# Kernel optimization log

Hardware: AMD Instinct MI355X
Metric: run time of the kernel (lower is better)

The kernel has to match this reference:

```python
import jax, jax.numpy as jnp
import numpy as np

H = 256          # hidden_channels
R = 64           # num_rbf
N = 20000        # nodes
E = 320000       # edges
CUTOFF_LO = 0.0
CUTOFF_UP = 5.0
LN_EPS = 1e-5


def _layernorm(x, g, b):
    mu = jnp.mean(x, axis=-1, keepdims=True)
    var = jnp.var(x, axis=-1, keepdims=True)
    return (x - mu) * jax.lax.rsqrt(var + LN_EPS) * g + b


def _cosine_cutoff(r):
    # cutoff_lower == 0 branch of CosineCutoff
    c = 0.5 * (jnp.cos(r * (jnp.pi / CUTOFF_UP)) + 1.0)
    return c * (r < CUTOFF_UP).astype(r.dtype)


def setup_inputs() -> dict:
    key = jax.random.key(0)
    ks = jax.random.split(key, 16)
    def xavier(k, shape):
        fan_in, fan_out = shape[1], shape[0]
        lim = np.sqrt(6.0 / (fan_in + fan_out))
        return jax.random.uniform(k, shape, jnp.float32, -lim, lim)
    x = jax.random.normal(ks[0], (N, H), jnp.float32)
    edge_index = jax.random.randint(ks[1], (2, E), 0, N, jnp.int64)
    edge_weight = jax.random.uniform(ks[2], (E,), jnp.float32, 0.0, CUTOFF_UP)
    edge_attr = jax.random.normal(ks[3], (E, R), jnp.float32)
    return {
        "x": x,
        "edge_index": edge_index,
        "edge_weight": edge_weight,
        "edge_attr": edge_attr,
        "ln_g": jnp.ones((H,), jnp.float32),
        "ln_b": jnp.zeros((H,), jnp.float32),
        "Wq": xavier(ks[4], (H, H)), "bq": jnp.zeros((H,), jnp.float32),
        "Wk": xavier(ks[5], (H, H)), "bk": jnp.zeros((H,), jnp.float32),
        "Wv": xavier(ks[6], (H, H)), "bv": jnp.zeros((H,), jnp.float32),
        "Wo": xavier(ks[7], (H, H)), "bo": jnp.zeros((H,), jnp.float32),
        "Wdk": xavier(ks[8], (H, R)), "bdk": jnp.zeros((H,), jnp.float32),
        "Wdv": xavier(ks[9], (H, R)), "bdv": jnp.zeros((H,), jnp.float32),
    }


def reference(x, edge_index, edge_weight, edge_attr,
              ln_g, ln_b, Wq, bq, Wk, bk, Wv, bv, Wo, bo, Wdk, bdk, Wdv, bdv):
    src = edge_index[0]  # j (messages come from)
    dst = edge_index[1]  # i (messages aggregate to)

    x_norm = _layernorm(x, ln_g, ln_b)                     # [N,H]
    q = x_norm @ Wq.T + bq                                 # [N,H]
    k = x_norm @ Wk.T + bk
    v = x_norm @ Wv.T + bv

    dk = jax.nn.silu(edge_attr @ Wdk.T + bdk)              # [E,H]
    dv = jax.nn.silu(edge_attr @ Wdv.T + bdv)              # [E,H]

    q_i = q[dst]                                           # [E,H]
    k_j = k[src]
    v_j = v[src]

    attn = jnp.sum(q_i * k_j * dk, axis=1)                 # [E]
    attn = jax.nn.silu(attn) * _cosine_cutoff(edge_weight) # [E]

    msg = v_j * dv * attn[:, None]                         # [E,H]
    agg = jax.ops.segment_sum(msg, dst, num_segments=x.shape[0])  # [N,H]

    out = agg @ Wo.T + bo
    return x + out
```

## Files before the change

### kernel.cpp

```cpp
#include <hip/hip_runtime.h>
#include <math.h>

#define NN 20000
#define H 256
#define R 64
#define EE 320000
#define LN_EPS 1e-5f
#define NB 79

using short8  = __attribute__((ext_vector_type(8))) short;
using ushort8 = __attribute__((ext_vector_type(8))) unsigned short;
using f32x4   = __attribute__((ext_vector_type(4))) float;

typedef __attribute__((address_space(3))) unsigned int lds_uint;
typedef const __attribute__((address_space(1))) unsigned int glb_uint;

__device__ __forceinline__ float silu_f(float x) {
    return x * __builtin_amdgcn_rcpf(1.0f + __expf(-x));
}

__device__ __forceinline__ unsigned short f2bf(float f) {
    unsigned u = __float_as_uint(f);
    u += 0x7fff + ((u >> 16) & 1);
    return (unsigned short)(u >> 16);
}
__device__ __forceinline__ float bf2f(unsigned short s) {
    return __uint_as_float(((unsigned)s) << 16);
}
__device__ __forceinline__ unsigned short f2h(float f) {
    unsigned r;
    asm("v_cvt_f16_f32 %0, %1" : "=v"(r) : "v"(f));
    return (unsigned short)r;
}
__device__ __forceinline__ float h2f(unsigned short h) {
    float f;
    asm("v_cvt_f32_f16 %0, %1" : "=v"(f) : "v"((unsigned)h));
    return f;
}

__device__ __forceinline__ int sw_idx(int row, int col) {
    return row * 64 + ((((col >> 3) ^ (row & 7)) << 3) | (col & 7));
}
__device__ __forceinline__ int dh_idx(int row, int col) {
    return row * 256 + (col ^ (((row >> 2) & 3) << 4));
}

__global__ __launch_bounds__(256) void k_prep(
    const float* __restrict__ Wq, const float* __restrict__ Wk,
    const float* __restrict__ Wv, const float* __restrict__ Wo,
    const float* __restrict__ g,  const float* __restrict__ b,
    const float* __restrict__ bq, const float* __restrict__ bk, const float* __restrict__ bv,
    const float* __restrict__ Wdk, const float* __restrict__ Wdv,
    unsigned short* __restrict__ wqkv_p, unsigned short* __restrict__ wo_p,
    unsigned short* __restrict__ wdk_p,  unsigned short* __restrict__ wdv_p,
    float* __restrict__ bias3, int* __restrict__ hist)
{
    const int bid = blockIdx.x, t = threadIdx.x;
    if (bid < 128) {
        const int mat = bid >> 5;
        const float* W = mat == 0 ? Wq : (mat == 1 ? Wk : (mat == 2 ? Wv : Wo));
        unsigned short* out = (mat < 3) ? wqkv_p + (size_t)mat * 131072 : wo_p;
        const int fold = mat < 3;
        const int flat = (bid & 31) * 256 + t;
        const int tile = flat >> 9;
        const int rem  = flat & 511;
        const int ks   = rem >> 6;
        const int lane = rem & 63;
        const int nl = lane & 15, quad = lane >> 4;
        const int h  = tile * 16 + nl;
        const int c0 = ks * 32 + quad * 8;
        short8 hi8, lo8;
        #pragma unroll
        for (int j = 0; j < 8; ++j) {
            float wv = W[(size_t)h * 256 + c0 + j];
            if (fold) wv *= g[c0 + j];
            const unsigned short hh = f2bf(wv);
            hi8[j] = (short)hh;
            lo8[j] = (short)f2bf(wv - bf2f(hh));
        }
        unsigned short* ob = out + ((size_t)(tile * 8 + ks)) * 1024;
        *(short8*)&ob[lane * 8] = hi8;
        *(short8*)&ob[512 + lane * 8] = lo8;
    } else if (bid < 160) {
        const int flat = (bid - 128) * 256 + t;
        const int mat  = flat >> 12;
        const int rem  = flat & 4095;
        const int hh   = rem >> 11;
        const int r2   = rem & 2047;
        const int row  = r2 >> 4;
        const int col4 = (r2 & 15) * 4;
        const float* W = mat == 0 ? Wdk : Wdv;
        unsigned short* out = (mat == 0 ? wdk_p : wdv_p) + hh * 16384;
        const float4 w4 = *(const float4*)(W + (size_t)(hh * 128 + row) * 64 + col4);
        const unsigned short h0 = f2bf(w4.x), h1 = f2bf(w4.y), h2 = f2bf(w4.z), h3 = f2bf(w4.w);
        ushort4 hi4 = {h0, h1, h2, h3};
        ushort4 lo4 = {f2bf(w4.x - bf2f(h0)), f2bf(w4.y - bf2f(h1)),
                       f2bf(w4.z - bf2f(h2)), f2bf(w4.w - bf2f(h3))};
        const int di = sw_idx(row, col4);
        *(ushort4*)&out[di] = hi4;
        *(ushort4*)&out[8192 + di] = lo4;
    } else if (bid < 163) {
        const int mat = bid - 160, h = t;
        const float* W  = mat == 0 ? Wq : (mat == 1 ? Wk : Wv);
        const float* bb = mat == 0 ? bq : (mat == 1 ? bk : bv);
        float s = 0.f;
        const float* wr = W + (size_t)h * 256;
        for (int c = 0; c < 256; c += 4) {
            const float4 w4 = *(const float4*)(wr + c);
            const float4 b4 = *(const float4*)(b + c);
            s += w4.x * b4.x + w4.y * b4.y + w4.z * b4.z + w4.w * b4.w;
        }
        bias3[mat * 256 + h] = bb[h] + s;
    } else {
        const int i = (bid - 163) * 256 + t;
        if (i < NN) hist[i] = 0;
    }
}

__global__ __launch_bounds__(64, 2) void k_ln_qkv(
    const float* __restrict__ x,
    const unsigned short* __restrict__ wqkv_p, const float* __restrict__ bias3,
    float* __restrict__ q, float* __restrict__ k, float* __restrict__ v)
{
    const int t = threadIdx.x;
    const int lane = t & 63;
    const int nl = lane & 15, quad = lane >> 4;
    const int nbase = blockIdx.x * 16;
    const int node = nbase + nl;
    const bool nv = node < NN;

    float xv[64];
    float sum = 0.f, sq = 0.f;
    {
        const float* xp = x + (size_t)node * H + quad * 8;
        #pragma unroll
        for (int ks = 0; ks < 8; ++ks) {
            float4 x0 = {0.f,0.f,0.f,0.f}, x1 = {0.f,0.f,0.f,0.f};
            if (nv) {
                x0 = *(const float4*)(xp + ks * 32);
                x1 = *(const float4*)(xp + ks * 32 + 4);
            }
            xv[ks*8+0]=x0.x; xv[ks*8+1]=x0.y; xv[ks*8+2]=x0.z; xv[ks*8+3]=x0.w;
            xv[ks*8+4]=x1.x; xv[ks*8+5]=x1.y; xv[ks*8+6]=x1.z; xv[ks*8+7]=x1.w;
            sum += x0.x+x0.y+x0.z+x0.w + x1.x+x1.y+x1.z+x1.w;
            sq  += x0.x*x0.x+x0.y*x0.y+x0.z*x0.z+x0.w*x0.w
                 + x1.x*x1.x+x1.y*x1.y+x1.z*x1.z+x1.w*x1.w;
        }
    }
    sum += __shfl_xor(sum, 16); sum += __shfl_xor(sum, 32);
    sq  += __shfl_xor(sq, 16);  sq  += __shfl_xor(sq, 32);
    const float mu  = sum * (1.0f / H);
    const float var = sq * (1.0f / H) - mu * mu;
    const float rs  = rsqrtf(var + LN_EPS);

    short8 a_hi[8], a_lo[8];
    #pragma unroll
    for (int ks = 0; ks < 8; ++ks) {
        #pragma unroll
        for (int j = 0; j < 8; ++j) {
            const float z = (xv[ks*8+j] - mu) * rs;
            const unsigned short hh = f2bf(z);
            a_hi[ks][j] = (short)hh;
            a_lo[ks][j] = (short)f2bf(z - bf2f(hh));
        }
    }

    for (int mat = 0; mat < 3; ++mat) {
        float* outp = mat == 0 ? q : (mat == 1 ? k : v);
        const float* bp = bias3 + mat * 256;
        const unsigned short* wb = wqkv_p + (size_t)mat * 131072 + lane * 8;
        for (int tile = 0; tile < 16; ++tile) {
            const unsigned short* gb = wb + (size_t)tile * 8192;
            const float bbv = bp[tile * 16 + nl];
            f32x4 acc = {bbv, bbv, bbv, bbv};
            #pragma unroll
            for (int ks = 0; ks < 8; ++ks) {
                const short8 b_hi = *(const short8*)(gb + ks * 1024);
                const short8 b_lo = *(const short8*)(gb + ks * 1024 + 512);
                acc = __builtin_amdgcn_mfma_f32_16x16x32_bf16(a_hi[ks], b_hi, acc, 0, 0, 0);
                acc = __builtin_amdgcn_mfma_f32_16x16x32_bf16(a_lo[ks], b_hi, acc, 0, 0, 0);
                acc = __builtin_amdgcn_mfma_f32_16x16x32_bf16(a_hi[ks], b_lo, acc, 0, 0, 0);
            }
            #pragma unroll
            for (int r = 0; r < 4; ++r) {
                const int onode = nbase + quad * 4 + r;
                if (onode < NN)
                    outp[(size_t)onode * H + tile * 16 + nl] = acc[r];
            }
        }
    }
}

__global__ __launch_bounds__(256) void k_hist(const int* __restrict__ ei, int* __restrict__ hist) {
    int e = blockIdx.x * 256 + threadIdx.x;
    if (e < EE) atomicAdd(&hist[ei[EE + e]], 1);
}

__global__ __launch_bounds__(256) void k_scan1(const int* __restrict__ hist,
                                               int* __restrict__ cursor, int* __restrict__ bsum) {
    const int t = threadIdx.x, i = blockIdx.x * 256 + t;
    const int lane = t & 63, w = t >> 6;
    const int v = (i < NN) ? hist[i] : 0;
    int incl = v;
    #pragma unroll
    for (int off = 1; off < 64; off <<= 1) {
        int u = __shfl_up(incl, off);
        if (lane >= off) incl += u;
    }
    __shared__ int ws[4];
    if (lane == 63) ws[w] = incl;
    __syncthreads();
    int base = 0;
    #pragma unroll
    for (int j = 0; j < 4; ++j) if (j < w) base += ws[j];
    if (i < NN) cursor[i] = base + incl - v;
    if (t == 255) bsum[blockIdx.x] = base + incl;
}

__global__ __launch_bounds__(128) void k_scan2(int* __restrict__ bsum) {
    __shared__ int buf[128];
    const int t = threadIdx.x;
    const int v = (t < NB) ? bsum[t] : 0;
    buf[t] = v;
    __syncthreads();
    #pragma unroll
    for (int off = 1; off < 128; off <<= 1) {
        int add = (t >= off) ? buf[t - off] : 0;
        __syncthreads();
        buf[t] += add;
        __syncthreads();
    }
    if (t < NB) bsum[t] = buf[t] - v;
}

__global__ __launch_bounds__(256) void k_scatter(const int* __restrict__ ei,
                                                 int* __restrict__ cursor,
                                                 const int* __restrict__ bsum,
                                                 int* __restrict__ perm) {
    int e = blockIdx.x * 256 + threadIdx.x;
    if (e < EE) {
        int d = ei[EE + e];
        int pos = atomicAdd(&cursor[d], 1) + bsum[d >> 8];
        perm[pos] = e;
    }
}

__global__ __launch_bounds__(256, 2) void k_edge(
    const float* __restrict__ q, const float* __restrict__ k, const float* __restrict__ v,
    const int* __restrict__ ei, const float* __restrict__ ew, const float* __restrict__ ea,
    const unsigned short* __restrict__ wdk_p, const float* __restrict__ bdk,
    const unsigned short* __restrict__ wdv_p, const float* __restrict__ bdv,
    const int* __restrict__ perm,
    float* __restrict__ agg)
{
    __shared__ __align__(16) unsigned short w_region[2 * 128 * 64];
    __shared__ __align__(16) unsigned short dks_h[64 * 256];
    __shared__ float attn_s[64];
    __shared__ int src_s[64], dst_s[64];

    const unsigned short* w_hi_s = w_region;
    const unsigned short* w_lo_s = w_region + 128 * 64;

    const int t    = threadIdx.x;
    const int bi   = blockIdx.x;
    const int eb   = ((bi & 7) * 625 + (bi >> 3)) * 64;
    const int lane = t & 63, wave = t >> 6;
    const int nl   = lane & 15, quad = lane >> 4;
    const int estrip = wave * 16;
    const int tx = t & 31, ty = t >> 5;
    const int h0 = tx * 4, e0 = ty * 8;

    {
        const ushort8* sp = (const ushort8*)wdk_p + t;
        ushort8* dpw = (ushort8*)w_region + (t & 192);
        #pragma unroll
        for (int c = 0; c < 8; ++c)
            __builtin_amdgcn_global_load_lds((glb_uint*)(sp + c * 256),
                                             (lds_uint*)(dpw + c * 256), 16, 0, 0);
    }

    if (t < 64) {
        const int e = perm[eb + t];
        src_s[t] = ei[e];
        dst_s[t] = ei[EE + e];
        attn_s[t] = 0.f;
    }

    short8 a_hi[2], a_lo[2];
    {
        const int e = perm[eb + estrip + nl];
        const float* ap = ea + (size_t)e * R + quad * 8;
        #pragma unroll
        for (int ks = 0; ks < 2; ++ks) {
            const f32x4 x0 = *(const f32x4*)(ap + ks * 32);
            const f32x4 x1 = *(const f32x4*)(ap + ks * 32 + 4);
            const float zz[8] = {x0[0], x0[1], x0[2], x0[3], x1[0], x1[1], x1[2], x1[3]};
            #pragma unroll
            for (int j = 0; j < 8; ++j) {
                const unsigned short hv = f2bf(zz[j]);
                a_hi[ks][j] = (short)hv;
                a_lo[ks][j] = (short)f2bf(zz[j] - bf2f(hv));
            }
        }
    }
    __syncthreads();

    #define MFMA_TO_DKS(BIAS, HALF)                                                   \
    {                                                                                 \
        f32x4 accA[8];                                                                \
        _Pragma("unroll")                                                             \
        for (int tt = 0; tt < 8; ++tt) {                                              \
            const int wrow = tt * 16 + nl;                                            \
            short8 b_hi[2], b_lo[2];                                                  \
            _Pragma("unroll")                                                         \
            for (int ks = 0; ks < 2; ++ks) {                                          \
                const int idx = wrow * 64 + ((((ks * 4 + quad) ^ (nl & 7)) << 3));    \
                b_hi[ks] = *(const short8*)&w_hi_s[idx];                              \
                b_lo[ks] = *(const short8*)&w_lo_s[idx];                              \
            }                                                                         \
            const float bb = (BIAS)[(HALF) * 128 + tt * 16 + nl];                     \
            f32x4 acc = {bb, bb, bb, bb};                                             \
            _Pragma("unroll")                                                         \
            for (int ks = 0; ks < 2; ++ks) {                                          \
                acc = __builtin_amdgcn_mfma_f32_16x16x32_bf16(a_hi[ks], b_hi[ks], acc, 0, 0, 0); \
                acc = __builtin_amdgcn_mfma_f32_16x16x32_bf16(a_lo[ks], b_hi[ks], acc, 0, 0, 0); \
                acc = __builtin_amdgcn_mfma_f32_16x16x32_bf16(a_hi[ks], b_lo[ks], acc, 0, 0, 0); \
            }                                                                         \
            accA[tt] = acc;                                                           \
        }                                                                             \
        __syncthreads();                         \
                   \
        _Pragma("unroll")                                                             \
        for (int tt = 0; tt < 8; ++tt)                                                \
            _Pragma("unroll")                                                         \
            for (int r = 0; r < 4; ++r)                                               \
                dks_h[dh_idx(estrip + quad * 4 + r, (HALF) * 128 + tt * 16 + nl)] =   \
                    f2h(silu_f(accA[tt][r]));                                         \
    }

    #define STAGE(PTR)                                                                \
    {                                                                                 \
        const ushort8* sp = (const ushort8*)(PTR) + t;                                \
        ushort8* dpw = (ushort8*)w_region + (t & 192);                                \
        _Pragma("unroll")                                                             \
        for (int c = 0; c < 8; ++c)                                                   \
            __builtin_amdgcn_global_load_lds((glb_uint*)(sp + c * 256),               \
                                             (lds_uint*)(dpw + c * 256), 16, 0, 0);   \
    }

    {
        f32x4 accA[8];
        #pragma unroll
        for (int tt = 0; tt < 8; ++tt) {
            const int wrow = tt * 16 + nl;
            short8 b_hi[2], b_lo[2];
            #pragma unroll
            for (int ks = 0; ks < 2; ++ks) {
                const int idx = wrow * 64 + ((((ks * 4 + quad) ^ (nl & 7)) << 3));
                b_hi[ks] = *(const short8*)&w_hi_s[idx];
                b_lo[ks] = *(const short8*)&w_lo_s[idx];
            }
            const float bb = bdk[tt * 16 + nl];
            f32x4 acc = {bb, bb, bb, bb};
            #pragma unroll
            for (int ks = 0; ks < 2; ++ks) {
                acc = __builtin_amdgcn_mfma_f32_16x16x32_bf16(a_hi[ks], b_hi[ks], acc, 0, 0, 0);
                acc = __builtin_amdgcn_mfma_f32_16x16x32_bf16(a_lo[ks], b_hi[ks], acc, 0, 0, 0);
                acc = __builtin_amdgcn_mfma_f32_16x16x32_bf16(a_hi[ks], b_lo[ks], acc, 0, 0, 0);
            }
            accA[tt] = acc;
        }
        __syncthreads();
        STAGE(wdk_p + 16384);
        #pragma unroll
        for (int tt = 0; tt < 8; ++tt)
            #pragma unroll
            for (int r = 0; r < 4; ++r)
                dks_h[dh_idx(estrip + quad * 4 + r, tt * 16 + nl)] =
                    f2h(silu_f(accA[tt][r]));
    }
    __syncthreads();
    MFMA_TO_DKS(bdk, 1);
    STAGE(wdv_p);

    {
        float4 qi0 = {0.f,0.f,0.f,0.f}, qi1 = {0.f,0.f,0.f,0.f};
        int pd = -1;
        #pragma unroll
        for (int i = 0; i < 8; ++i) {
            const int d = dst_s[e0 + i], s = src_s[e0 + i];
            if (d != pd) {
                qi0 = *(const float4*)(q + (size_t)d * H + h0);
                qi1 = *(const float4*)(q + (size_t)d * H + 128 + h0);
                pd = d;
            }
            const float4 kj0 = *(const float4*)(k + (size_t)s * H + h0);
            const float4 kj1 = *(const float4*)(k + (size_t)s * H + 128 + h0);
            const ushort4 d40 = *(const ushort4*)&dks_h[dh_idx(e0 + i, h0)];
            const ushort4 d41 = *(const ushort4*)&dks_h[dh_idx(e0 + i, 128 + h0)];
            float part = qi0.x * kj0.x * h2f(d40.x) + qi0.y * kj0.y * h2f(d40.y)
                       + qi0.z * kj0.z * h2f(d40.z) + qi0.w * kj0.w * h2f(d40.w)
                       + qi1.x * kj1.x * h2f(d41.x) + qi1.y * kj1.y * h2f(d41.y)
                       + qi1.z * kj1.z * h2f(d41.z) + qi1.w * kj1.w * h2f(d41.w);
            #pragma unroll
            for (int off = 16; off; off >>= 1) part += __shfl_xor(part, off);
            if (tx == 0) attn_s[e0 + i] += part;
        }
    }
    __syncthreads();

    if (t < 64) {
        const int e = perm[eb + t];
        const float rr = ew[e];
        const float cut = (rr < 5.0f) ? 0.5f * (__cosf(rr * 0.6283185307f) + 1.0f) : 0.0f;
        attn_s[t] = silu_f(attn_s[t]) * cut;
    }

    MFMA_TO_DKS(bdv, 0);
    STAGE(wdv_p + 16384);
    __syncthreads();
    MFMA_TO_DKS(bdv, 1);

    {
        float4 m0 = {0.f,0.f,0.f,0.f}, m1 = {0.f,0.f,0.f,0.f};
        int cur_d = -1;
        #pragma unroll
        for (int i = 0; i < 8; ++i) {
            const int d = dst_s[e0 + i], s = src_s[e0 + i];
            const float a = attn_s[e0 + i];
            const float4 vj0 = *(const float4*)(v + (size_t)s * H + h0);
            const float4 vj1 = *(const float4*)(v + (size_t)s * H + 128 + h0);
            const ushort4 d40 = *(const ushort4*)&dks_h[dh_idx(e0 + i, h0)];
            const ushort4 d41 = *(const ushort4*)&dks_h[dh_idx(e0 + i, 128 + h0)];
            if (d != cur_d) {
                if (cur_d >= 0) {
                    float* dp = agg + (size_t)cur_d * H;
                    atomicAdd(dp + h0 + 0, m0.x); atomicAdd(dp + h0 + 1, m0.y);
                    atomicAdd(dp + h0 + 2, m0.z); atomicAdd(dp + h0 + 3, m0.w);
                    atomicAdd(dp + 128 + h0 + 0, m1.x); atomicAdd(dp + 128 + h0 + 1, m1.y);
                    atomicAdd(dp + 128 + h0 + 2, m1.z); atomicAdd(dp + 128 + h0 + 3, m1.w);
                }
                m0.x = vj0.x * h2f(d40.x) * a; m0.y = vj0.y * h2f(d40.y) * a;
                m0.z = vj0.z * h2f(d40.z) * a; m0.w = vj0.w * h2f(d40.w) * a;
                m1.x = vj1.x * h2f(d41.x) * a; m1.y = vj1.y * h2f(d41.y) * a;
                m1.z = vj1.z * h2f(d41.z) * a; m1.w = vj1.w * h2f(d41.w) * a;
                cur_d = d;
            } else {
                m0.x += vj0.x * h2f(d40.x) * a; m0.y += vj0.y * h2f(d40.y) * a;
                m0.z += vj0.z * h2f(d40.z) * a; m0.w += vj0.w * h2f(d40.w) * a;
                m1.x += vj1.x * h2f(d41.x) * a; m1.y += vj1.y * h2f(d41.y) * a;
                m1.z += vj1.z * h2f(d41.z) * a; m1.w += vj1.w * h2f(d41.w) * a;
            }
        }
        {
            float* dp = agg + (size_t)cur_d * H;
            atomicAdd(dp + h0 + 0, m0.x); atomicAdd(dp + h0 + 1, m0.y);
            atomicAdd(dp + h0 + 2, m0.z); atomicAdd(dp + h0 + 3, m0.w);
            atomicAdd(dp + 128 + h0 + 0, m1.x); atomicAdd(dp + 128 + h0 + 1, m1.y);
            atomicAdd(dp + 128 + h0 + 2, m1.z); atomicAdd(dp + 128 + h0 + 3, m1.w);
        }
    }
    #undef MFMA_TO_DKS
    #undef STAGE
}

__global__ __launch_bounds__(64, 2) void k_out(
    const float* __restrict__ aggm, const unsigned short* __restrict__ wo_p,
    const float* __restrict__ bo, const float* __restrict__ x, float* __restrict__ out)
{
    const int t = threadIdx.x;
    const int lane = t & 63;
    const int nl = lane & 15, quad = lane >> 4;
    const int nbase = blockIdx.x * 16;
    const int node = nbase + nl;
    const bool nv = node < NN;

    short8 a_hi[8], a_lo[8];
    {
        const float* ap = aggm + (size_t)node * H + quad * 8;
        #pragma unroll
        for (int ks = 0; ks < 8; ++ks) {
            float4 x0 = {0.f,0.f,0.f,0.f}, x1 = {0.f,0.f,0.f,0.f};
            if (nv) { x0 = *(const float4*)(ap + ks * 32); x1 = *(const float4*)(ap + ks * 32 + 4); }
            const float zz[8] = {x0.x,x0.y,x0.z,x0.w,x1.x,x1.y,x1.z,x1.w};
            #pragma unroll
            for (int j = 0; j < 8; ++j) {
                const unsigned short hh = f2bf(zz[j]);
                a_hi[ks][j] = (short)hh;
                a_lo[ks][j] = (short)f2bf(zz[j] - bf2f(hh));
            }
        }
    }
    for (int tile = 0; tile < 16; ++tile) {
        const unsigned short* gb = wo_p + (size_t)tile * 8192 + lane * 8;
        const float bbv = bo[tile * 16 + nl];
        f32x4 acc = {bbv, bbv, bbv, bbv};
        #pragma unroll
        for (int ks = 0; ks < 8; ++ks) {
            const short8 b_hi = *(const short8*)(gb + ks * 1024);
            const short8 b_lo = *(const short8*)(gb + ks * 1024 + 512);
            acc = __builtin_amdgcn_mfma_f32_16x16x32_bf16(a_hi[ks], b_hi, acc, 0, 0, 0);
            acc = __builtin_amdgcn_mfma_f32_16x16x32_bf16(a_lo[ks], b_hi, acc, 0, 0, 0);
            acc = __builtin_amdgcn_mfma_f32_16x16x32_bf16(a_hi[ks], b_lo, acc, 0, 0, 0);
        }
        #pragma unroll
        for (int r = 0; r < 4; ++r) {
            const int onode = nbase + quad * 4 + r;
            if (onode < NN) {
                const size_t oi = (size_t)onode * H + tile * 16 + nl;
                out[oi] = x[oi] + acc[r];
            }
        }
    }
}

extern "C" void kernel_launch(void* const* d_in, const int* in_sizes, int n_in,
                              void* d_out, int out_size, void* d_ws, size_t ws_size,
                              hipStream_t stream) {
    const float* x   = (const float*)d_in[0];
    const int*   ei  = (const int*)d_in[1];
    const float* ew  = (const float*)d_in[2];
    const float* ea  = (const float*)d_in[3];
    const float* g   = (const float*)d_in[4];
    const float* b   = (const float*)d_in[5];
    const float* Wq  = (const float*)d_in[6];  const float* bq  = (const float*)d_in[7];
    const float* Wk  = (const float*)d_in[8];  const float* bk  = (const float*)d_in[9];
    const float* Wv  = (const float*)d_in[10]; const float* bv  = (const float*)d_in[11];
    const float* Wo  = (const float*)d_in[12]; const float* bo  = (const float*)d_in[13];
    const float* Wdk = (const float*)d_in[14]; const float* bdk = (const float*)d_in[15];
    const float* Wdv = (const float*)d_in[16]; const float* bdv = (const float*)d_in[17];

    float* q    = (float*)d_ws;
    float* k    = q + (size_t)NN * H;
    float* v    = k + (size_t)NN * H;
    float* agg  = v + (size_t)NN * H;
    int*   hist = (int*)(agg + (size_t)NN * H);
    int*   cur  = hist + NN;
    int*   bsum = cur + NN;
    int*   perm = bsum + 128;
    unsigned short* wqkv_p = (unsigned short*)(perm + EE);
    unsigned short* wo_p   = wqkv_p + 393216;
    unsigned short* wdk_p  = wo_p + 131072;
    unsigned short* wdv_p  = wdk_p + 32768;
    float* bias3 = (float*)(wdv_p + 32768);

    hipMemsetAsync(agg, 0, (size_t)NN * H * sizeof(float), stream);
    k_prep<<<242, 256, 0, stream>>>(Wq, Wk, Wv, Wo, g, b, bq, bk, bv, Wdk, Wdv,
                                    wqkv_p, wo_p, wdk_p, wdv_p, bias3, hist);
    k_hist<<<EE / 256, 256, 0, stream>>>(ei, hist);
    k_ln_qkv<<<(NN + 15) / 16, 64, 0, stream>>>(x, wqkv_p, bias3, q, k, v);
    k_scan1<<<NB, 256, 0, stream>>>(hist, cur, bsum);
    k_scan2<<<1, 128, 0, stream>>>(bsum);
    k_scatter<<<EE / 256, 256, 0, stream>>>(ei, cur, bsum, perm);
    k_edge<<<EE / 64, 256, 0, stream>>>(q, k, v, ei, ew, ea, wdk_p, bdk, wdv_p, bdv, perm, agg);
    k_out<<<(NN + 15) / 16, 64, 0, stream>>>(agg, wo_p, bo, x, (float*)d_out);
}
```

Baseline: 630.1 us.

## Store q/k/v in fp16 and prefetch gathers early in edge kernel

```diff
diff --git a/kernel.cpp b/kernel.cpp
--- a/kernel.cpp
+++ b/kernel.cpp
@@ -11,6 +11,7 @@
 using short8  = __attribute__((ext_vector_type(8))) short;
 using ushort8 = __attribute__((ext_vector_type(8))) unsigned short;
 using f32x4   = __attribute__((ext_vector_type(4))) float;
+using half8   = __attribute__((ext_vector_type(8))) _Float16;
 
 typedef __attribute__((address_space(3))) unsigned int lds_uint;
 typedef const __attribute__((address_space(1))) unsigned int glb_uint;
@@ -31,11 +32,6 @@
     unsigned r;
     asm("v_cvt_f16_f32 %0, %1" : "=v"(r) : "v"(f));
     return (unsigned short)r;
-}
-__device__ __forceinline__ float h2f(unsigned short h) {
-    float f;
-    asm("v_cvt_f32_f16 %0, %1" : "=v"(f) : "v"((unsigned)h));
-    return f;
 }
 
 __device__ __forceinline__ int sw_idx(int row, int col) {
@@ -120,7 +116,8 @@
 __global__ __launch_bounds__(64, 2) void k_ln_qkv(
     const float* __restrict__ x,
     const unsigned short* __restrict__ wqkv_p, const float* __restrict__ bias3,
-    float* __restrict__ q, float* __restrict__ k, float* __restrict__ v)
+    unsigned short* __restrict__ q, unsigned short* __restrict__ k,
+    unsigned short* __restrict__ v)
 {
     const int t = threadIdx.x;
     const int lane = t & 63;
@@ -166,7 +163,7 @@
     }
 
     for (int mat = 0; mat < 3; ++mat) {
-        float* outp = mat == 0 ? q : (mat == 1 ? k : v);
+        unsigned short* outp = mat == 0 ? q : (mat == 1 ? k : v);
         const float* bp = bias3 + mat * 256;
         const unsigned short* wb = wqkv_p + (size_t)mat * 131072 + lane * 8;
         for (int tile = 0; tile < 16; ++tile) {
@@ -185,7 +182,7 @@
             for (int r = 0; r < 4; ++r) {
                 const int onode = nbase + quad * 4 + r;
                 if (onode < NN)
-                    outp[(size_t)onode * H + tile * 16 + nl] = acc[r];
+                    outp[(size_t)onode * H + tile * 16 + nl] = f2h(acc[r]);
             }
         }
     }
@@ -246,7 +243,8 @@
 }
 
 __global__ __launch_bounds__(256, 2) void k_edge(
-    const float* __restrict__ q, const float* __restrict__ k, const float* __restrict__ v,
+    const unsigned short* __restrict__ q16, const unsigned short* __restrict__ k16,
+    const unsigned short* __restrict__ v16,
     const int* __restrict__ ei, const float* __restrict__ ew, const float* __restrict__ ea,
     const unsigned short* __restrict__ wdk_p, const float* __restrict__ bdk,
     const unsigned short* __restrict__ wdv_p, const float* __restrict__ bdv,
@@ -268,42 +266,17 @@
     const int nl   = lane & 15, quad = lane >> 4;
     const int estrip = wave * 16;
     const int tx = t & 31, ty = t >> 5;
-    const int h0 = tx * 4, e0 = ty * 8;
-
-    {
-        const ushort8* sp = (const ushort8*)wdk_p + t;
-        ushort8* dpw = (ushort8*)w_region + (t & 192);
-        #pragma unroll
-        for (int c = 0; c < 8; ++c)
-            __builtin_amdgcn_global_load_lds((glb_uint*)(sp + c * 256),
-                                             (lds_uint*)(dpw + c * 256), 16, 0, 0);
-    }
-
-    if (t < 64) {
-        const int e = perm[eb + t];
-        src_s[t] = ei[e];
-        dst_s[t] = ei[EE + e];
-        attn_s[t] = 0.f;
-    }
-
-    short8 a_hi[2], a_lo[2];
-    {
-        const int e = perm[eb + estrip + nl];
-        const float* ap = ea + (size_t)e * R + quad * 8;
-        #pragma unroll
-        for (int ks = 0; ks < 2; ++ks) {
-            const f32x4 x0 = *(const f32x4*)(ap + ks * 32);
-            const f32x4 x1 = *(const f32x4*)(ap + ks * 32 + 4);
-            const float zz[8] = {x0[0], x0[1], x0[2], x0[3], x1[0], x1[1], x1[2], x1[3]};
-            #pragma unroll
-            for (int j = 0; j < 8; ++j) {
-                const unsigned short hv = f2bf(zz[j]);
-                a_hi[ks][j] = (short)hv;
-                a_lo[ks][j] = (short)f2bf(zz[j] - bf2f(hv));
-            }
-        }
-    }
-    __syncthreads();
+    const int c8 = tx * 8, e0 = ty * 8;
+
+    #define STAGE(PTR)                                                                \
+    {                                                                                 \
+        const ushort8* sp = (const ushort8*)(PTR) + t;                                \
+        ushort8* dpw = (ushort8*)w_region + (t & 192);                                \
+        _Pragma("unroll")                                                             \
+        for (int c = 0; c < 8; ++c)                                                   \
+            __builtin_amdgcn_global_load_lds((glb_uint*)(sp + c * 256),               \
+                                             (lds_uint*)(dpw + c * 256), 16, 0, 0);   \
+    }
 
     #define MFMA_TO_DKS(BIAS, HALF)                                                   \
     {                                                                                 \
@@ -329,7 +302,6 @@
             accA[tt] = acc;                                                           \
         }                                                                             \
         __syncthreads();                         \
-                   \
         _Pragma("unroll")                                                             \
         for (int tt = 0; tt < 8; ++tt)                                                \
             _Pragma("unroll")                                                         \
@@ -338,14 +310,39 @@
                     f2h(silu_f(accA[tt][r]));                                         \
     }
 
-    #define STAGE(PTR)                                                                \
-    {                                                                                 \
-        const ushort8* sp = (const ushort8*)(PTR) + t;                                \
-        ushort8* dpw = (ushort8*)w_region + (t & 192);                                \
-        _Pragma("unroll")                                                             \
-        for (int c = 0; c < 8; ++c)                                                   \
-            __builtin_amdgcn_global_load_lds((glb_uint*)(sp + c * 256),               \
-                                             (lds_uint*)(dpw + c * 256), 16, 0, 0);   \
+    STAGE(wdk_p);
+
+    if (t < 64) {
+        const int e = perm[eb + t];
+        src_s[t] = ei[e];
+        dst_s[t] = ei[EE + e];
+    }
+
+    short8 a_hi[2], a_lo[2];
+    {
+        const int e = perm[eb + estrip + nl];
+        const float* ap = ea + (size_t)e * R + quad * 8;
+        #pragma unroll
+        for (int ks = 0; ks < 2; ++ks) {
+            const f32x4 x0 = *(const f32x4*)(ap + ks * 32);
+            const f32x4 x1 = *(const f32x4*)(ap + ks * 32 + 4);
+            const float zz[8] = {x0[0], x0[1], x0[2], x0[3], x1[0], x1[1], x1[2], x1[3]};
+            #pragma unroll
+            for (int j = 0; j < 8; ++j) {
+                const unsigned short hv = f2bf(zz[j]);
+                a_hi[ks][j] = (short)hv;
+                a_lo[ks][j] = (short)f2bf(zz[j] - bf2f(hv));
+            }
+        }
+    }
+    __syncthreads();
+
+    half8 kj8[8], qi8[8];
+    #pragma unroll
+    for (int i = 0; i < 8; ++i) {
+        const int s = src_s[e0 + i], d = dst_s[e0 + i];
+        kj8[i] = *(const half8*)(k16 + (size_t)s * H + c8);
+        qi8[i] = *(const half8*)(q16 + (size_t)d * H + c8);
     }
 
     {
@@ -383,30 +380,24 @@
     MFMA_TO_DKS(bdk, 1);
     STAGE(wdv_p);
 
-    {
-        float4 qi0 = {0.f,0.f,0.f,0.f}, qi1 = {0.f,0.f,0.f,0.f};
-        int pd = -1;
-        #pragma unroll
-        for (int i = 0; i < 8; ++i) {
-            const int d = dst_s[e0 + i], s = src_s[e0 + i];
-            if (d != pd) {
-                qi0 = *(const float4*)(q + (size_t)d * H + h0);
-                qi1 = *(const float4*)(q + (size_t)d * H + 128 + h0);
-                pd = d;
-            }
-            const float4 kj0 = *(const float4*)(k + (size_t)s * H + h0);
-            const float4 kj1 = *(const float4*)(k + (size_t)s * H + 128 + h0);
-            const ushort4 d40 = *(const ushort4*)&dks_h[dh_idx(e0 + i, h0)];
-            const ushort4 d41 = *(const ushort4*)&dks_h[dh_idx(e0 + i, 128 + h0)];
-            float part = qi0.x * kj0.x * h2f(d40.x) + qi0.y * kj0.y * h2f(d40.y)
-                       + qi0.z * kj0.z * h2f(d40.z) + qi0.w * kj0.w * h2f(d40.w)
-                       + qi1.x * kj1.x * h2f(d41.x) + qi1.y * kj1.y * h2f(d41.y)
-                       + qi1.z * kj1.z * h2f(d41.z) + qi1.w * kj1.w * h2f(d41.w);
-            #pragma unroll
-            for (int off = 16; off; off >>= 1) part += __shfl_xor(part, off);
-            if (tx == 0) attn_s[e0 + i] += part;
-        }
-    }
+    #pragma unroll
+    for (int i = 0; i < 8; ++i) {
+        const half8 qk = qi8[i] * kj8[i];
+        const half8 dd = *(const half8*)&dks_h[dh_idx(e0 + i, c8)];
+        float part = 0.f;
+        #pragma unroll
+        for (int j = 0; j < 8; ++j)
+            part += (float)qk[j] * (float)dd[j];
+        #pragma unroll
+        for (int off = 16; off; off >>= 1) part += __shfl_xor(part, off);
+        if (tx == 0) attn_s[e0 + i] = part;
+    }
+
+    half8 vj8[8];
+    #pragma unroll
+    for (int i = 0; i < 8; ++i)
+        vj8[i] = *(const half8*)(v16 + (size_t)src_s[e0 + i] * H + c8);
+
     __syncthreads();
 
     if (t < 64) {
@@ -422,42 +413,31 @@
     MFMA_TO_DKS(bdv, 1);
 
     {
-        float4 m0 = {0.f,0.f,0.f,0.f}, m1 = {0.f,0.f,0.f,0.f};
+        float m[8] = {0.f,0.f,0.f,0.f,0.f,0.f,0.f,0.f};
         int cur_d = -1;
         #pragma unroll
         for (int i = 0; i < 8; ++i) {
-            const int d = dst_s[e0 + i], s = src_s[e0 + i];
+            const int d = dst_s[e0 + i];
             const float a = attn_s[e0 + i];
-            const float4 vj0 = *(const float4*)(v + (size_t)s * H + h0);
-            const float4 vj1 = *(const float4*)(v + (size_t)s * H + 128 + h0);
-            const ushort4 d40 = *(const ushort4*)&dks_h[dh_idx(e0 + i, h0)];
-            const ushort4 d41 = *(const ushort4*)&dks_h[dh_idx(e0 + i, 128 + h0)];
+            const half8 vd = vj8[i] * *(const half8*)&dks_h[dh_idx(e0 + i, c8)];
             if (d != cur_d) {
                 if (cur_d >= 0) {
-                    float* dp = agg + (size_t)cur_d * H;
-                    atomicAdd(dp + h0 + 0, m0.x); atomicAdd(dp + h0 + 1, m0.y);
-                    atomicAdd(dp + h0 + 2, m0.z); atomicAdd(dp + h0 + 3, m0.w);
-                    atomicAdd(dp + 128 + h0 + 0, m1.x); atomicAdd(dp + 128 + h0 + 1, m1.y);
-                    atomicAdd(dp + 128 + h0 + 2, m1.z); atomicAdd(dp + 128 + h0 + 3, m1.w);
+                    float* dp = agg + (size_t)cur_d * H + c8;
+                    #pragma unroll
+                    for (int j = 0; j < 8; ++j) atomicAdd(dp + j, m[j]);
                 }
-                m0.x = vj0.x * h2f(d40.x) * a; m0.y = vj0.y * h2f(d40.y) * a;
-                m0.z = vj0.z * h2f(d40.z) * a; m0.w = vj0.w * h2f(d40.w) * a;
-                m1.x = vj1.x * h2f(d41.x) * a; m1.y = vj1.y * h2f(d41.y) * a;
-                m1.z = vj1.z * h2f(d41.z) * a; m1.w = vj1.w * h2f(d41.w) * a;
+                #pragma unroll
+                for (int j = 0; j < 8; ++j) m[j] = (float)vd[j] * a;
                 cur_d = d;
             } else {
-                m0.x += vj0.x * h2f(d40.x) * a; m0.y += vj0.y * h2f(d40.y) * a;
-                m0.z += vj0.z * h2f(d40.z) * a; m0.w += vj0.w * h2f(d40.w) * a;
-                m1.x += vj1.x * h2f(d41.x) * a; m1.y += vj1.y * h2f(d41.y) * a;
-                m1.z += vj1.z * h2f(d41.z) * a; m1.w += vj1.w * h2f(d41.w) * a;
+                #pragma unroll
+                for (int j = 0; j < 8; ++j) m[j] += (float)vd[j] * a;
             }
         }
         {
-            float* dp = agg + (size_t)cur_d * H;
-            atomicAdd(dp + h0 + 0, m0.x); atomicAdd(dp + h0 + 1, m0.y);
-            atomicAdd(dp + h0 + 2, m0.z); atomicAdd(dp + h0 + 3, m0.w);
-            atomicAdd(dp + 128 + h0 + 0, m1.x); atomicAdd(dp + 128 + h0 + 1, m1.y);
-            atomicAdd(dp + 128 + h0 + 2, m1.z); atomicAdd(dp + 128 + h0 + 3, m1.w);
+            float* dp = agg + (size_t)cur_d * H + c8;
+            #pragma unroll
+            for (int j = 0; j < 8; ++j) atomicAdd(dp + j, m[j]);
         }
     }
     #undef MFMA_TO_DKS
@@ -530,10 +510,10 @@
     const float* Wdk = (const float*)d_in[14]; const float* bdk = (const float*)d_in[15];
     const float* Wdv = (const float*)d_in[16]; const float* bdv = (const float*)d_in[17];
 
-    float* q    = (float*)d_ws;
-    float* k    = q + (size_t)NN * H;
-    float* v    = k + (size_t)NN * H;
-    float* agg  = v + (size_t)NN * H;
+    unsigned short* q16 = (unsigned short*)d_ws;
+    unsigned short* k16 = q16 + (size_t)NN * H;
+    unsigned short* v16 = k16 + (size_t)NN * H;
+    float* agg  = (float*)(v16 + (size_t)NN * H);
     int*   hist = (int*)(agg + (size_t)NN * H);
     int*   cur  = hist + NN;
     int*   bsum = cur + NN;
@@ -548,10 +528,10 @@
     k_prep<<<242, 256, 0, stream>>>(Wq, Wk, Wv, Wo, g, b, bq, bk, bv, Wdk, Wdv,
                                     wqkv_p, wo_p, wdk_p, wdv_p, bias3, hist);
     k_hist<<<EE / 256, 256, 0, stream>>>(ei, hist);
-    k_ln_qkv<<<(NN + 15) / 16, 64, 0, stream>>>(x, wqkv_p, bias3, q, k, v);
+    k_ln_qkv<<<(NN + 15) / 16, 64, 0, stream>>>(x, wqkv_p, bias3, q16, k16, v16);
     k_scan1<<<NB, 256, 0, stream>>>(hist, cur, bsum);
     k_scan2<<<1, 128, 0, stream>>>(bsum);
     k_scatter<<<EE / 256, 256, 0, stream>>>(ei, cur, bsum, perm);
-    k_edge<<<EE / 64, 256, 0, stream>>>(q, k, v, ei, ew, ea, wdk_p, bdk, wdv_p, bdv, perm, agg);
+    k_edge<<<EE / 64, 256, 0, stream>>>(q16, k16, v16, ei, ew, ea, wdk_p, bdk, wdv_p, bdv, perm, agg);
     k_out<<<(NN + 15) / 16, 64, 0, stream>>>(agg, wo_p, bo, x, (float*)d_out);
 }
```

Result: slower. 796.9 us (+26.5%).

## Store q/k/v as fp16 and pre-sort src/dst/edge weights in scatter

Applied to the files above, without the earlier changes.

```diff
diff --git a/kernel.cpp b/kernel.cpp
--- a/kernel.cpp
+++ b/kernel.cpp
@@ -120,7 +120,8 @@
 __global__ __launch_bounds__(64, 2) void k_ln_qkv(
     const float* __restrict__ x,
     const unsigned short* __restrict__ wqkv_p, const float* __restrict__ bias3,
-    float* __restrict__ q, float* __restrict__ k, float* __restrict__ v)
+    unsigned short* __restrict__ q, unsigned short* __restrict__ k,
+    unsigned short* __restrict__ v)
 {
     const int t = threadIdx.x;
     const int lane = t & 63;
@@ -166,7 +167,7 @@
     }
 
     for (int mat = 0; mat < 3; ++mat) {
-        float* outp = mat == 0 ? q : (mat == 1 ? k : v);
+        unsigned short* outp = mat == 0 ? q : (mat == 1 ? k : v);
         const float* bp = bias3 + mat * 256;
         const unsigned short* wb = wqkv_p + (size_t)mat * 131072 + lane * 8;
         for (int tile = 0; tile < 16; ++tile) {
@@ -185,7 +186,7 @@
             for (int r = 0; r < 4; ++r) {
                 const int onode = nbase + quad * 4 + r;
                 if (onode < NN)
-                    outp[(size_t)onode * H + tile * 16 + nl] = acc[r];
+                    outp[(size_t)onode * H + tile * 16 + nl] = f2h(acc[r]);
             }
         }
     }
@@ -234,23 +235,33 @@
 }
 
 __global__ __launch_bounds__(256) void k_scatter(const int* __restrict__ ei,
+                                                 const float* __restrict__ ew,
                                                  int* __restrict__ cursor,
                                                  const int* __restrict__ bsum,
-                                                 int* __restrict__ perm) {
+                                                 int* __restrict__ perm,
+                                                 int* __restrict__ srcs,
+                                                 int* __restrict__ dsts,
+                                                 float* __restrict__ ews) {
     int e = blockIdx.x * 256 + threadIdx.x;
     if (e < EE) {
+        int s = ei[e];
         int d = ei[EE + e];
         int pos = atomicAdd(&cursor[d], 1) + bsum[d >> 8];
         perm[pos] = e;
+        srcs[pos] = s;
+        dsts[pos] = d;
+        ews[pos] = ew[e];
     }
 }
 
 __global__ __launch_bounds__(256, 2) void k_edge(
-    const float* __restrict__ q, const float* __restrict__ k, const float* __restrict__ v,
-    const int* __restrict__ ei, const float* __restrict__ ew, const float* __restrict__ ea,
+    const unsigned short* __restrict__ q16, const unsigned short* __restrict__ k16,
+    const unsigned short* __restrict__ v16,
+    const float* __restrict__ ea,
     const unsigned short* __restrict__ wdk_p, const float* __restrict__ bdk,
     const unsigned short* __restrict__ wdv_p, const float* __restrict__ bdv,
-    const int* __restrict__ perm,
+    const int* __restrict__ perm, const int* __restrict__ srcs,
+    const int* __restrict__ dsts, const float* __restrict__ ews,
     float* __restrict__ agg)
 {
     __shared__ __align__(16) unsigned short w_region[2 * 128 * 64];
@@ -270,40 +281,15 @@
     const int tx = t & 31, ty = t >> 5;
     const int h0 = tx * 4, e0 = ty * 8;
 
-    {
-        const ushort8* sp = (const ushort8*)wdk_p + t;
-        ushort8* dpw = (ushort8*)w_region + (t & 192);
-        #pragma unroll
-        for (int c = 0; c < 8; ++c)
-            __builtin_amdgcn_global_load_lds((glb_uint*)(sp + c * 256),
-                                             (lds_uint*)(dpw + c * 256), 16, 0, 0);
-    }
-
-    if (t < 64) {
-        const int e = perm[eb + t];
-        src_s[t] = ei[e];
-        dst_s[t] = ei[EE + e];
-        attn_s[t] = 0.f;
-    }
-
-    short8 a_hi[2], a_lo[2];
-    {
-        const int e = perm[eb + estrip + nl];
-        const float* ap = ea + (size_t)e * R + quad * 8;
-        #pragma unroll
-        for (int ks = 0; ks < 2; ++ks) {
-            const f32x4 x0 = *(const f32x4*)(ap + ks * 32);
-            const f32x4 x1 = *(const f32x4*)(ap + ks * 32 + 4);
-            const float zz[8] = {x0[0], x0[1], x0[2], x0[3], x1[0], x1[1], x1[2], x1[3]};
-            #pragma unroll
-            for (int j = 0; j < 8; ++j) {
-                const unsigned short hv = f2bf(zz[j]);
-                a_hi[ks][j] = (short)hv;
-                a_lo[ks][j] = (short)f2bf(zz[j] - bf2f(hv));
-            }
-        }
-    }
-    __syncthreads();
+    #define STAGE(PTR)                                                                \
+    {                                                                                 \
+        const ushort8* sp = (const ushort8*)(PTR) + t;                                \
+        ushort8* dpw = (ushort8*)w_region + (t & 192);                                \
+        _Pragma("unroll")                                                             \
+        for (int c = 0; c < 8; ++c)                                                   \
+            __builtin_amdgcn_global_load_lds((glb_uint*)(sp + c * 256),               \
+                                             (lds_uint*)(dpw + c * 256), 16, 0, 0);   \
+    }
 
     #define MFMA_TO_DKS(BIAS, HALF)                                                   \
     {                                                                                 \
@@ -329,7 +315,6 @@
             accA[tt] = acc;                                                           \
         }                                                                             \
         __syncthreads();                         \
-                   \
         _Pragma("unroll")                                                             \
         for (int tt = 0; tt < 8; ++tt)                                                \
             _Pragma("unroll")                                                         \
@@ -338,15 +323,32 @@
                     f2h(silu_f(accA[tt][r]));                                         \
     }
 
-    #define STAGE(PTR)                                                                \
-    {                                                                                 \
-        const ushort8* sp = (const ushort8*)(PTR) + t;                                \
-        ushort8* dpw = (ushort8*)w_region + (t & 192);                                \
-        _Pragma("unroll")                                                             \
-        for (int c = 0; c < 8; ++c)                                                   \
-            __builtin_amdgcn_global_load_lds((glb_uint*)(sp + c * 256),               \
-                                             (lds_uint*)(dpw + c * 256), 16, 0, 0);   \
-    }
+    STAGE(wdk_p);
+
+    if (t < 64) {
+        src_s[t] = srcs[eb + t];
+        dst_s[t] = dsts[eb + t];
+        attn_s[t] = 0.f;
+    }
+
+    short8 a_hi[2], a_lo[2];
+    {
+        const int e = perm[eb + estrip + nl];
+        const float* ap = ea + (size_t)e * R + quad * 8;
+        #pragma unroll
+        for (int ks = 0; ks < 2; ++ks) {
+            const f32x4 x0 = *(const f32x4*)(ap + ks * 32);
+            const f32x4 x1 = *(const f32x4*)(ap + ks * 32 + 4);
+            const float zz[8] = {x0[0], x0[1], x0[2], x0[3], x1[0], x1[1], x1[2], x1[3]};
+            #pragma unroll
+            for (int j = 0; j < 8; ++j) {
+                const unsigned short hv = f2bf(zz[j]);
+                a_hi[ks][j] = (short)hv;
+                a_lo[ks][j] = (short)f2bf(zz[j] - bf2f(hv));
+            }
+        }
+    }
+    __syncthreads();
 
     {
         f32x4 accA[8];
@@ -384,24 +386,26 @@
     STAGE(wdv_p);
 
     {
-        float4 qi0 = {0.f,0.f,0.f,0.f}, qi1 = {0.f,0.f,0.f,0.f};
+        float qv[8];
         int pd = -1;
         #pragma unroll
         for (int i = 0; i < 8; ++i) {
             const int d = dst_s[e0 + i], s = src_s[e0 + i];
             if (d != pd) {
-                qi0 = *(const float4*)(q + (size_t)d * H + h0);
-                qi1 = *(const float4*)(q + (size_t)d * H + 128 + h0);
+                const ushort4 q0 = *(const ushort4*)(q16 + (size_t)d * H + h0);
+                const ushort4 q1 = *(const ushort4*)(q16 + (size_t)d * H + 128 + h0);
+                qv[0] = h2f(q0.x); qv[1] = h2f(q0.y); qv[2] = h2f(q0.z); qv[3] = h2f(q0.w);
+                qv[4] = h2f(q1.x); qv[5] = h2f(q1.y); qv[6] = h2f(q1.z); qv[7] = h2f(q1.w);
                 pd = d;
             }
-            const float4 kj0 = *(const float4*)(k + (size_t)s * H + h0);
-            const float4 kj1 = *(const float4*)(k + (size_t)s * H + 128 + h0);
+            const ushort4 k0 = *(const ushort4*)(k16 + (size_t)s * H + h0);
+            const ushort4 k1 = *(const ushort4*)(k16 + (size_t)s * H + 128 + h0);
             const ushort4 d40 = *(const ushort4*)&dks_h[dh_idx(e0 + i, h0)];
             const ushort4 d41 = *(const ushort4*)&dks_h[dh_idx(e0 + i, 128 + h0)];
-            float part = qi0.x * kj0.x * h2f(d40.x) + qi0.y * kj0.y * h2f(d40.y)
-                       + qi0.z * kj0.z * h2f(d40.z) + qi0.w * kj0.w * h2f(d40.w)
-                       + qi1.x * kj1.x * h2f(d41.x) + qi1.y * kj1.y * h2f(d41.y)
-                       + qi1.z * kj1.z * h2f(d41.z) + qi1.w * kj1.w * h2f(d41.w);
+            float part = qv[0] * h2f(k0.x) * h2f(d40.x) + qv[1] * h2f(k0.y) * h2f(d40.y)
+                       + qv[2] * h2f(k0.z) * h2f(d40.z) + qv[3] * h2f(k0.w) * h2f(d40.w)
+                       + qv[4] * h2f(k1.x) * h2f(d41.x) + qv[5] * h2f(k1.y) * h2f(d41.y)
+                       + qv[6] * h2f(k1.z) * h2f(d41.z) + qv[7] * h2f(k1.w) * h2f(d41.w);
             #pragma unroll
             for (int off = 16; off; off >>= 1) part += __shfl_xor(part, off);
             if (tx == 0) attn_s[e0 + i] += part;
@@ -410,8 +414,7 @@
     __syncthreads();
 
     if (t < 64) {
-        const int e = perm[eb + t];
-        const float rr = ew[e];
+        const float rr = ews[eb + t];
         const float cut = (rr < 5.0f) ? 0.5f * (__cosf(rr * 0.6283185307f) + 1.0f) : 0.0f;
         attn_s[t] = silu_f(attn_s[t]) * cut;
     }
@@ -428,10 +431,14 @@
         for (int i = 0; i < 8; ++i) {
             const int d = dst_s[e0 + i], s = src_s[e0 + i];
             const float a = attn_s[e0 + i];
-            const float4 vj0 = *(const float4*)(v + (size_t)s * H + h0);
-            const float4 vj1 = *(const float4*)(v + (size_t)s * H + 128 + h0);
+            const ushort4 v0 = *(const ushort4*)(v16 + (size_t)s * H + h0);
+            const ushort4 v1 = *(const ushort4*)(v16 + (size_t)s * H + 128 + h0);
             const ushort4 d40 = *(const ushort4*)&dks_h[dh_idx(e0 + i, h0)];
             const ushort4 d41 = *(const ushort4*)&dks_h[dh_idx(e0 + i, 128 + h0)];
+            const float w0x = h2f(v0.x) * h2f(d40.x) * a, w0y = h2f(v0.y) * h2f(d40.y) * a;
+            const float w0z = h2f(v0.z) * h2f(d40.z) * a, w0w = h2f(v0.w) * h2f(d40.w) * a;
+            const float w1x = h2f(v1.x) * h2f(d41.x) * a, w1y = h2f(v1.y) * h2f(d41.y) * a;
+            const float w1z = h2f(v1.z) * h2f(d41.z) * a, w1w = h2f(v1.w) * h2f(d41.w) * a;
             if (d != cur_d) {
                 if (cur_d >= 0) {
                     float* dp = agg + (size_t)cur_d * H;
@@ -440,16 +447,12 @@
                     atomicAdd(dp + 128 + h0 + 0, m1.x); atomicAdd(dp + 128 + h0 + 1, m1.y);
                     atomicAdd(dp + 128 + h0 + 2, m1.z); atomicAdd(dp + 128 + h0 + 3, m1.w);
                 }
-                m0.x = vj0.x * h2f(d40.x) * a; m0.y = vj0.y * h2f(d40.y) * a;
-                m0.z = vj0.z * h2f(d40.z) * a; m0.w = vj0.w * h2f(d40.w) * a;
-                m1.x = vj1.x * h2f(d41.x) * a; m1.y = vj1.y * h2f(d41.y) * a;
-                m1.z = vj1.z * h2f(d41.z) * a; m1.w = vj1.w * h2f(d41.w) * a;
+                m0.x = w0x; m0.y = w0y; m0.z = w0z; m0.w = w0w;
+                m1.x = w1x; m1.y = w1y; m1.z = w1z; m1.w = w1w;
                 cur_d = d;
             } else {
-                m0.x += vj0.x * h2f(d40.x) * a; m0.y += vj0.y * h2f(d40.y) * a;
-                m0.z += vj0.z * h2f(d40.z) * a; m0.w += vj0.w * h2f(d40.w) * a;
-                m1.x += vj1.x * h2f(d41.x) * a; m1.y += vj1.y * h2f(d41.y) * a;
-                m1.z += vj1.z * h2f(d41.z) * a; m1.w += vj1.w * h2f(d41.w) * a;
+                m0.x += w0x; m0.y += w0y; m0.z += w0z; m0.w += w0w;
+                m1.x += w1x; m1.y += w1y; m1.z += w1z; m1.w += w1w;
             }
         }
         {
@@ -530,15 +533,18 @@
     const float* Wdk = (const float*)d_in[14]; const float* bdk = (const float*)d_in[15];
     const float* Wdv = (const float*)d_in[16]; const float* bdv = (const float*)d_in[17];
 
-    float* q    = (float*)d_ws;
-    float* k    = q + (size_t)NN * H;
-    float* v    = k + (size_t)NN * H;
-    float* agg  = v + (size_t)NN * H;
+    unsigned short* q16 = (unsigned short*)d_ws;
+    unsigned short* k16 = q16 + (size_t)NN * H;
+    unsigned short* v16 = k16 + (size_t)NN * H;
+    float* agg  = (float*)(v16 + (size_t)NN * H);
     int*   hist = (int*)(agg + (size_t)NN * H);
     int*   cur  = hist + NN;
     int*   bsum = cur + NN;
     int*   perm = bsum + 128;
-    unsigned short* wqkv_p = (unsigned short*)(perm + EE);
+    int*   srcs = perm + EE;
+    int*   dsts = srcs + EE;
+    float* ews  = (float*)(dsts + EE);
+    unsigned short* wqkv_p = (unsigned short*)(ews + EE);
     unsigned short* wo_p   = wqkv_p + 393216;
     unsigned short* wdk_p  = wo_p + 131072;
     unsigned short* wdv_p  = wdk_p + 32768;
@@ -548,10 +554,11 @@
     k_prep<<<242, 256, 0, stream>>>(Wq, Wk, Wv, Wo, g, b, bq, bk, bv, Wdk, Wdv,
                                     wqkv_p, wo_p, wdk_p, wdv_p, bias3, hist);
     k_hist<<<EE / 256, 256, 0, stream>>>(ei, hist);
-    k_ln_qkv<<<(NN + 15) / 16, 64, 0, stream>>>(x, wqkv_p, bias3, q, k, v);
+    k_ln_qkv<<<(NN + 15) / 16, 64, 0, stream>>>(x, wqkv_p, bias3, q16, k16, v16);
     k_scan1<<<NB, 256, 0, stream>>>(hist, cur, bsum);
     k_scan2<<<1, 128, 0, stream>>>(bsum);
-    k_scatter<<<EE / 256, 256, 0, stream>>>(ei, cur, bsum, perm);
-    k_edge<<<EE / 64, 256, 0, stream>>>(q, k, v, ei, ew, ea, wdk_p, bdk, wdv_p, bdv, perm, agg);
+    k_scatter<<<EE / 256, 256, 0, stream>>>(ei, ew, cur, bsum, perm, srcs, dsts, ews);
+    k_edge<<<EE / 64, 256, 0, stream>>>(q16, k16, v16, ea, wdk_p, bdk, wdv_p, bdv,
+                                        perm, srcs, dsts, ews, agg);
     k_out<<<(NN + 15) / 16, 64, 0, stream>>>(agg, wo_p, bo, x, (float*)d_out);
 }
```

Result: no change. 635.3 us (+0.8%).
